# Performance work log

Hardware: AMD Instinct MI355X
Metric: run time of the kernel (lower is better)

Reference implementation:

```python
import jax, jax.numpy as jnp
import numpy as np

N = 3000
NFEAT = 512
NHID1 = 64
NHID2 = 32
FUS = 64
NCLASS = 8
NHEADS = 4
NADJ = 2
ALPHA = 0.2
NEG = -9e15


def setup_inputs() -> dict:
    key = jax.random.key(0)
    ks = jax.random.split(key, 14)
    s = 0.1
    return dict(
        x=jax.random.normal(ks[0], (N, NFEAT), jnp.float32),
        adj=jax.random.randint(ks[1], (NADJ, N, N), 0, 2, jnp.int32),
        W1=jax.random.normal(ks[2], (NADJ, NHEADS, NFEAT, NHID1), jnp.float32) * s,
        a1=jax.random.normal(ks[3], (NADJ, NHEADS, 2 * NHID1), jnp.float32) * s,
        W2=jax.random.normal(ks[4], (NADJ, NHEADS, FUS, NHID2), jnp.float32) * s,
        a2=jax.random.normal(ks[5], (NADJ, NHEADS, 2 * NHID2), jnp.float32) * s,
        wint1=jax.random.normal(ks[6], (FUS, NHID1 * NHEADS), jnp.float32) * s,
        bint1=jax.random.normal(ks[7], (FUS,), jnp.float32) * s,
        wfus1=jax.random.normal(ks[8], (FUS, FUS * NADJ), jnp.float32) * s,
        bfus1=jax.random.normal(ks[9], (FUS,), jnp.float32) * s,
        wint2=jax.random.normal(ks[10], (NCLASS, NHID2 * NHEADS), jnp.float32) * s,
        bint2=jax.random.normal(ks[11], (NCLASS,), jnp.float32) * s,
        wfus2=jax.random.normal(ks[12], (NCLASS, NCLASS * NADJ), jnp.float32) * s,
        bfus2=jax.random.normal(ks[13], (NCLASS,), jnp.float32) * s,
    )


def _gat(h, adj, W, a):
    # h: [N,F] shared input; W: [A,H,F,O]; a: [A,H,2O]; adj: [A,N,N]
    O = W.shape[-1]
    Wh = jnp.einsum('nf,ahfo->ahno', h, W)                 # [A,H,N,O]
    f1 = jnp.einsum('ahno,aho->ahn', Wh, a[..., :O])
    f2 = jnp.einsum('ahno,aho->ahn', Wh, a[..., O:])
    e = jax.nn.leaky_relu(f1[:, :, :, None] + f2[:, :, None, :], ALPHA)
    e = jnp.where(adj[:, None, :, :] > 0, e, NEG)          # masked scores
    att = jax.nn.softmax(e, axis=-1)                       # row softmax
    hp = jax.nn.elu(jnp.einsum('ahnm,ahmo->ahno', att, Wh))
    A, H, n, o = hp.shape
    return hp.transpose(0, 2, 1, 3).reshape(A, n, H * o)   # head concat: [A,N,H*O]


def reference(x, adj, W1, a1, W2, a2, wint1, bint1, wfus1, bfus1,
              wint2, bint2, wfus2, bfus2):
    # stage 1 (dropout is identity in eval mode)
    h1 = _gat(x, adj, W1, a1)                                      # [A,N,H*NHID1]
    h1 = jax.nn.elu(jnp.einsum('anf,gf->ang', h1, wint1) + bint1)  # [A,N,FUS]
    h1 = h1.transpose(1, 0, 2).reshape(h1.shape[1], -1)            # [N,A*FUS]
    out = h1 @ wfus1.T + bfus1                                     # [N,FUS]
    l1a = jnp.mean(jnp.abs(wfus1))
    # stage 2
    h2 = _gat(out, adj, W2, a2)                                    # [A,N,H*NHID2]
    h2 = jax.nn.elu(jnp.einsum('anf,gf->ang', h2, wint2) + bint2)  # [A,N,NCLASS]
    h2 = h2.transpose(1, 0, 2).reshape(h2.shape[1], -1)            # [N,A*NCLASS]
    out2 = h2 @ wfus2.T + bfus2                                    # [N,NCLASS]
    l1b = jnp.mean(jnp.abs(wfus2))
    return jax.nn.log_softmax(out2, axis=1), l1a + l1b
```

## Files before the change

kernel.cpp:

```cpp
#include <hip/hip_runtime.h>
#include <hip/hip_bf16.h>
#include <math.h>

#define NNODE 3000
#define NCHUNK 47
#define NBPR 376
#define ALPHA 0.2f
#define LDT 3008
#define LOG2E 1.4426950408889634f

typedef __attribute__((ext_vector_type(8))) short short8v;
typedef __attribute__((ext_vector_type(4))) short short4v;
typedef __attribute__((ext_vector_type(4))) float float4v;

static __device__ __forceinline__ short f2b(float x) {
  __hip_bfloat16 b = __float2bfloat16(x);
  return *reinterpret_cast<short*>(&b);
}
static __device__ __forceinline__ float b2f(unsigned short u) {
  unsigned v = ((unsigned)u) << 16;
  return *reinterpret_cast<float*>(&v);
}

__global__ __launch_bounds__(256)
void k_bitmask(const int* __restrict__ adj, unsigned char* __restrict__ bmb) {
  int idx = blockIdx.x * 256 + threadIdx.x;
  if (idx >= 2 * NNODE * NBPR) return;
  int row = idx / NBPR, b = idx % NBPR;
  unsigned char v = 0;
  if (b < 375) {
    const int* p = adj + (size_t)row * NNODE + 8 * b;
    int4 a0 = *reinterpret_cast<const int4*>(p);
    int4 a1 = *reinterpret_cast<const int4*>(p + 4);
    v = (unsigned char)((a0.x > 0) | ((a0.y > 0) << 1) | ((a0.z > 0) << 2) |
                        ((a0.w > 0) << 3) | ((a1.x > 0) << 4) | ((a1.y > 0) << 5) |
                        ((a1.z > 0) << 6) | ((a1.w > 0) << 7));
  }
  bmb[idx] = v;
}

__global__ __launch_bounds__(256)
void k_cast(const float* __restrict__ src, unsigned short* __restrict__ dst,
            int count8) {
  int i = blockIdx.x * 256 + threadIdx.x;
  if (i >= count8) return;
  float4 va = reinterpret_cast<const float4*>(src)[2 * i];
  float4 vb = reinterpret_cast<const float4*>(src)[2 * i + 1];
  short8v w;
  w[0] = f2b(va.x); w[1] = f2b(va.y); w[2] = f2b(va.z); w[3] = f2b(va.w);
  w[4] = f2b(vb.x); w[5] = f2b(vb.y); w[6] = f2b(vb.z); w[7] = f2b(vb.w);
  reinterpret_cast<short8v*>(dst)[i] = w;
}

template <int O>
__global__ __launch_bounds__(256)
void k_wt(const float* __restrict__ src, unsigned short* __restrict__ dst,
          int rows, int ldT) {
  const int z = blockIdx.y;
  const int m0 = blockIdx.x * 64;
  src += (size_t)z * rows * O;
  dst += (size_t)z * O * ldT;
  __shared__ float Lw[64][O + 4];
  const int tid = threadIdx.x;
  for (int idx = tid; idx < 64 * (O / 4); idx += 256) {
    int m = idx / (O / 4), oc = idx % (O / 4);
    float4 v = make_float4(0.f, 0.f, 0.f, 0.f);
    if (m0 + m < rows)
      v = *reinterpret_cast<const float4*>(&src[(size_t)(m0 + m) * O + 4 * oc]);
    *reinterpret_cast<float4*>(&Lw[m][4 * oc]) = v;
  }
  __syncthreads();
  const int o = tid & (O - 1);
  for (int mc = tid / O; mc < 8; mc += 256 / O) {
    short8v w;
#pragma unroll
    for (int j = 0; j < 8; ++j) w[j] = f2b(Lw[8 * mc + j][o]);
    *reinterpret_cast<short8v*>(&dst[(size_t)o * ldT + m0 + 8 * mc]) = w;
  }
}

template <int OW, int KC, int MODE, int ACT>
__global__ __launch_bounds__(128)
void k_xw(const unsigned short* __restrict__ Ab, long long boffA,
          const unsigned short* __restrict__ Bb, long long boffB,
          const float* __restrict__ aux,
          unsigned short* __restrict__ Wo,
          long long boffW,
          float* __restrict__ f1o, float* __restrict__ f2o,
          int colStrideZ, int ldC) {
  constexpr int NCT = OW / 16;
  const int z = blockIdx.z;
  const int n0 = blockIdx.x * 32;
  const int ocol0 = blockIdx.y * OW;
  const unsigned short* A = Ab + boffA * z;
  const unsigned short* B = Bb + boffB * z;
  const int tid = threadIdx.x;
  const int l = tid & 63, g = l >> 4, li = l & 15;
  const int r0 = 16 * (tid >> 6);
  __shared__ __align__(16) unsigned short As[32 * 64];
  __shared__ __align__(16) unsigned short Bs[OW * 64];
  float4v acc[NCT];
#pragma unroll
  for (int ct = 0; ct < NCT; ++ct) acc[ct] = {0.f, 0.f, 0.f, 0.f};
  for (int k0 = 0; k0 < KC; k0 += 64) {
    for (int i = tid; i < 256; i += 128) {
      int r = i >> 3, c8 = i & 7;
      uint4 v = {0u, 0u, 0u, 0u};
      if (n0 + r < NNODE)
        v = *reinterpret_cast<const uint4*>(A + (size_t)(n0 + r) * KC + k0 + 8 * c8);
      int boff = (r * 128 + c8 * 16) ^ ((r & 7) << 4);
      *reinterpret_cast<uint4*>(reinterpret_cast<char*>(As) + boff) = v;
    }
    for (int i = tid; i < OW * 8; i += 128) {
      int ro = i >> 3, c8 = i & 7;
      uint4 v = *reinterpret_cast<const uint4*>(B + (size_t)(ocol0 + ro) * KC + k0 + 8 * c8);
      int boff = (ro * 128 + c8 * 16) ^ ((ro & 7) << 4);
      *reinterpret_cast<uint4*>(reinterpret_cast<char*>(Bs) + boff) = v;
    }
    __syncthreads();
#pragma unroll
    for (int q = 0; q < 2; ++q) {
      int aoff = ((r0 + li) * 128 + q * 64 + 16 * g) ^ ((li & 7) << 4);
      short8v afr = *reinterpret_cast<const short8v*>(
          reinterpret_cast<const char*>(As) + aoff);
#pragma unroll
      for (int ct = 0; ct < NCT; ++ct) {
        int orow = ct * 16 + li;
        int boff = (orow * 128 + q * 64 + 16 * g) ^ ((li & 7) << 4);
        short8v bfr = *reinterpret_cast<const short8v*>(
            reinterpret_cast<const char*>(Bs) + boff);
        acc[ct] = __builtin_amdgcn_mfma_f32_16x16x32_bf16(afr, bfr, acc[ct], 0, 0, 0);
      }
    }
    __syncthreads();
  }
  if (MODE == 1) {
    const float* av = aux + (size_t)z * 2 * OW;
    float p1[4] = {0.f, 0.f, 0.f, 0.f}, p2[4] = {0.f, 0.f, 0.f, 0.f};
#pragma unroll
    for (int ct = 0; ct < NCT; ++ct) {
      float a1v = av[ct * 16 + li];
      float a2v = av[OW + ct * 16 + li];
#pragma unroll
      for (int j = 0; j < 4; ++j) {
        p1[j] += acc[ct][j] * a1v;
        p2[j] += acc[ct][j] * a2v;
      }
    }
#pragma unroll
    for (int off = 1; off < 16; off <<= 1) {
#pragma unroll
      for (int j = 0; j < 4; ++j) {
        p1[j] += __shfl_xor(p1[j], off);
        p2[j] += __shfl_xor(p2[j], off);
      }
    }
    unsigned short* WT = Wo + boffW * z;
#pragma unroll
    for (int ct = 0; ct < NCT; ++ct) {
      short4v w;
#pragma unroll
      for (int j = 0; j < 4; ++j) w[j] = f2b(acc[ct][j]);
      *reinterpret_cast<short4v*>(
          &WT[(size_t)(ocol0 + ct * 16 + li) * LDT + n0 + r0 + 4 * g]) = w;
    }
    if (li == 0) {
#pragma unroll
      for (int j = 0; j < 4; ++j) {
        int n = n0 + r0 + 4 * g + j;
        if (n < NNODE) {
          f1o[(size_t)z * NNODE + n] = p1[j] * LOG2E;
          f2o[(size_t)z * NNODE + n] = p2[j] * LOG2E;
        }
      }
    }
  } else {
#pragma unroll
    for (int ct = 0; ct < NCT; ++ct) {
      float b = aux[ocol0 + ct * 16 + li];
#pragma unroll
      for (int j = 0; j < 4; ++j) {
        int n = n0 + r0 + 4 * g + j;
        if (n < NNODE) {
          float v = acc[ct][j] + b;
          if (ACT == 1) v = v > 0.f ? v : (__expf(v) - 1.f);
          Wo[(size_t)n * ldC + z * colStrideZ + ocol0 + ct * 16 + li] = (unsigned short)f2b(v);
        }
      }
    }
  }
}

template <int O, int CPS, bool PB16>
__global__ __launch_bounds__(256)
void k_pvp(const unsigned short* __restrict__ WhT,
           const float* __restrict__ f1, const float* __restrict__ f2,
           const unsigned long long* __restrict__ bm,
           void* __restrict__ Cpart, float* __restrict__ rsum) {
  constexpr int NCT = O / 16;
  const int z = blockIdx.z, a = z >> 2;
  const int ks = blockIdx.y;
  const int n0 = blockIdx.x * 64;
  const int kc0 = ks * CPS;
  const int nch = (NCHUNK - kc0 < CPS) ? (NCHUNK - kc0) : CPS;
  const int tid = threadIdx.x;
  const int l = tid & 63, li = l & 15, g = l >> 4;
  const int r0 = 16 * (tid >> 6);
  const unsigned short* WT = WhT + (size_t)z * O * LDT;
  const float* f2B = f2 + (size_t)z * NNODE;
  const unsigned long long* bmA = bm + (size_t)a * NNODE * NCHUNK;
  __shared__ __align__(16) unsigned short Whs[2][O * 64];
  __shared__ __align__(16) float F2d[2][64];
  __shared__ unsigned long long Bw2[2][64];
  __shared__ float F1s[64];
  if (tid < 64) {
    int n = n0 + tid;
    F1s[tid] = (n < NNODE) ? f1[(size_t)z * NNODE + n] : 0.f;
  }
  short8v onesf;
  {
    short ov = (li == 0) ? (short)0x3F80 : (short)0;
#pragma unroll
    for (int e = 0; e < 8; ++e) onesf[e] = ov;
  }
  auto stage = [&](int t, int buf) {
    if (tid < 64) {
      int n = n0 + tid;
      Bw2[buf][tid] = (n < NNODE) ? bmA[(size_t)n * NCHUNK + kc0 + t] : 0ULL;
    } else if (tid < 128) {
      int m = (kc0 + t) * 64 + (tid - 64);
      F2d[buf][tid - 64] = (m < NNODE) ? f2B[m] : 0.f;
    }
    for (int i = tid; i < O * 8; i += 256) {
      int ro = i >> 3, c8 = i & 7;
      uint4 v = *reinterpret_cast<const uint4*>(
          WT + (size_t)ro * LDT + (size_t)(kc0 + t) * 64 + 8 * c8);
      int boff = (ro * 128 + c8 * 16) ^ ((ro & 7) << 4);
      *reinterpret_cast<uint4*>(reinterpret_cast<char*>(Whs[buf]) + boff) = v;
    }
  };
  float4v acc[NCT];
#pragma unroll
  for (int ct = 0; ct < NCT; ++ct) acc[ct] = {0.f, 0.f, 0.f, 0.f};
  float4v accs = {0.f, 0.f, 0.f, 0.f};
  stage(0, 0);
  __syncthreads();
  for (int t = 0; t < nch; ++t) {
    int buf = t & 1;
    if (t + 1 < nch) stage(t + 1, buf ^ 1);
    const unsigned long long bwr = Bw2[buf][r0 + li];
    const float f1v = F1s[r0 + li];
    short8v afr[2];
#pragma unroll
    for (int q = 0; q < 2; ++q) {
      int koff = 32 * q + 8 * g;
      unsigned bits = (unsigned)(bwr >> koff) & 0xffu;
      const float4 fa = *reinterpret_cast<const float4*>(&F2d[buf][koff]);
      const float4 fb = *reinterpret_cast<const float4*>(&F2d[buf][koff + 4]);
      float f2v[8] = {fa.x, fa.y, fa.z, fa.w, fb.x, fb.y, fb.z, fb.w};
#pragma unroll
      for (int e = 0; e < 8; ++e) {
        float tt = f1v + f2v[e];
        tt = fmaxf(tt, ALPHA * tt);
        tt = (bits & (1u << e)) ? tt : -1.0e30f;
        afr[q][e] = f2b(__builtin_amdgcn_exp2f(tt));
      }
    }
#pragma unroll
    for (int ct = 0; ct < NCT; ++ct) {
      int orow = ct * 16 + li;
#pragma unroll
      for (int q = 0; q < 2; ++q) {
        int boff = (orow * 128 + q * 64 + 16 * g) ^ ((li & 7) << 4);
        short8v bfr = *reinterpret_cast<const short8v*>(
            reinterpret_cast<const char*>(Whs[buf]) + boff);
        acc[ct] = __builtin_amdgcn_mfma_f32_16x16x32_bf16(afr[q], bfr, acc[ct], 0, 0, 0);
      }
    }
    accs = __builtin_amdgcn_mfma_f32_16x16x32_bf16(afr[0], onesf, accs, 0, 0, 0);
    accs = __builtin_amdgcn_mfma_f32_16x16x32_bf16(afr[1], onesf, accs, 0, 0, 0);
    __syncthreads();
  }
  if (PB16) {
    unsigned short* Cp = (unsigned short*)Cpart + ((size_t)ks * 8 + z) * NNODE * O;
#pragma unroll
    for (int j = 0; j < 4; ++j) {
      int n = n0 + r0 + 4 * g + j;
      if (n < NNODE) {
#pragma unroll
        for (int ct = 0; ct < NCT; ++ct)
          Cp[(size_t)n * O + ct * 16 + li] = (unsigned short)f2b(acc[ct][j]);
      }
    }
  } else {
    float* Cp = (float*)Cpart + ((size_t)ks * 8 + z) * NNODE * O;
#pragma unroll
    for (int j = 0; j < 4; ++j) {
      int n = n0 + r0 + 4 * g + j;
      if (n < NNODE) {
#pragma unroll
        for (int ct = 0; ct < NCT; ++ct)
          Cp[(size_t)n * O + ct * 16 + li] = acc[ct][j];
      }
    }
  }
  if (li == 0) {
#pragma unroll
    for (int j = 0; j < 4; ++j) {
      int n = n0 + r0 + 4 * g + j;
      if (n < NNODE) rsum[((size_t)ks * 8 + z) * NNODE + n] = accs[j];
    }
  }
}

template <int O, int KS, bool PB16, bool WB16>
__global__ __launch_bounds__(256)
void k_pvred(const void* __restrict__ Cpart, const float* __restrict__ rsum,
             float* __restrict__ Cf, unsigned short* __restrict__ Cb) {
  constexpr int C4 = O / 4;
  int idx = blockIdx.x * 256 + threadIdx.x;
  if (idx >= 8 * NNODE * C4) return;
  int zn = idx / C4, c4 = idx % C4;
  int z = zn / NNODE, n = zn % NNODE;
  int a = z >> 2, h = z & 3;
  float s = 0.f;
#pragma unroll
  for (int k = 0; k < KS; ++k) s += rsum[(size_t)k * 8 * NNODE + zn];
  float inv = (s > 0.f) ? 1.f / s : 0.f;
  float accv[4] = {0.f, 0.f, 0.f, 0.f};
#pragma unroll
  for (int k = 0; k < KS; ++k) {
    if (PB16) {
      short4v v = *reinterpret_cast<const short4v*>(
          (const unsigned short*)Cpart + (size_t)k * 8 * NNODE * O + (size_t)zn * O + 4 * c4);
#pragma unroll
      for (int j = 0; j < 4; ++j) accv[j] += b2f((unsigned short)v[j]);
    } else {
      float4 v = *reinterpret_cast<const float4*>(
          (const float*)Cpart + (size_t)k * 8 * NNODE * O + (size_t)zn * O + 4 * c4);
      accv[0] += v.x; accv[1] += v.y; accv[2] += v.z; accv[3] += v.w;
    }
  }
  size_t base = ((size_t)a * NNODE + n) * (4 * O) + (size_t)h * O + 4 * c4;
  if (WB16) {
    short4v w;
#pragma unroll
    for (int j = 0; j < 4; ++j) {
      float v = accv[j] * inv;
      v = v > 0.f ? v : (__expf(v) - 1.f);
      w[j] = f2b(v);
    }
    *reinterpret_cast<short4v*>(Cb + base) = w;
  } else {
    float4 w;
    float* wp = &w.x;
#pragma unroll
    for (int j = 0; j < 4; ++j) {
      float v = accv[j] * inv;
      wp[j] = v > 0.f ? v : (__expf(v) - 1.f);
    }
    *reinterpret_cast<float4*>(Cf + base) = w;
  }
}

template <int BM, int BN, int BK, int TM, int TN, bool BT, int ACT>
__global__ __launch_bounds__((BM / TM) * (BN / TN))
void k_gemm(const float* __restrict__ A, long long boffA, int ldA,
            const float* __restrict__ B, long long boffB,
            const float* __restrict__ bias,
            float* __restrict__ C, long long boffC, int ldC,
            int M, int N, int K) {
  constexpr int NT = (BM / TM) * (BN / TN);
  constexpr int NCG = BN / TN;
  const int z = blockIdx.z;
  A += boffA * z;
  B += boffB * z;
  C += boffC * z;
  const int m0 = blockIdx.x * BM;
  const int n0 = blockIdx.y * BN;
  __shared__ float As[BK][BM + 4];
  __shared__ float Bs[BK][BN + 4];
  const int tid = threadIdx.x;
  const int trow = tid / NCG, tcol = tid % NCG;
  float acc[TM][TN] = {};
  for (int k0 = 0; k0 < K; k0 += BK) {
    for (int i = tid; i < BM * BK; i += NT) {
      int r = i / BK, c = i % BK;
      int gm = m0 + r;
      As[c][r] = (gm < M) ? A[(size_t)gm * ldA + (k0 + c)] : 0.f;
    }
    if (!BT) {
      for (int i = tid; i < BK * BN; i += NT) {
        int r = i / BN, c = i % BN;
        Bs[r][c] = B[(size_t)(k0 + r) * N + (n0 + c)];
      }
    } else {
      for (int i = tid; i < BK * BN; i += NT) {
        int r = i % BK, c = i / BK;
        Bs[r][c] = B[(size_t)(n0 + c) * K + (k0 + r)];
      }
    }
    __syncthreads();
#pragma unroll 8
    for (int kk = 0; kk < BK; ++kk) {
      float ar[TM], br[TN];
#pragma unroll
      for (int i2 = 0; i2 < TM; ++i2) ar[i2] = As[kk][trow * TM + i2];
#pragma unroll
      for (int j = 0; j < TN; ++j) br[j] = Bs[kk][tcol * TN + j];
#pragma unroll
      for (int i2 = 0; i2 < TM; ++i2)
#pragma unroll
        for (int j = 0; j < TN; ++j)
          acc[i2][j] = fmaf(ar[i2], br[j], acc[i2][j]);
    }
    __syncthreads();
  }
#pragma unroll
  for (int i2 = 0; i2 < TM; ++i2) {
    int gm = m0 + trow * TM + i2;
    if (gm >= M) continue;
#pragma unroll
    for (int j = 0; j < TN; ++j) {
      int gn = n0 + tcol * TN + j;
      float v = acc[i2][j];
      if (bias) v += bias[gn];
      if (ACT == 1) v = v > 0.f ? v : (__expf(v) - 1.f);
      C[(size_t)gm * ldC + gn] = v;
    }
  }
}

__global__ __launch_bounds__(256)
void k_lsm(const float* __restrict__ out2, float* __restrict__ out) {
  int n = blockIdx.x * blockDim.x + threadIdx.x;
  if (n >= NNODE) return;
  const float* r = out2 + (size_t)n * 8;
  float mx = r[0];
#pragma unroll
  for (int j = 1; j < 8; ++j) mx = fmaxf(mx, r[j]);
  float s = 0.f;
#pragma unroll
  for (int j = 0; j < 8; ++j) s += __expf(r[j] - mx);
  float ls = __logf(s) + mx;
#pragma unroll
  for (int j = 0; j < 8; ++j) out[(size_t)n * 8 + j] = r[j] - ls;
}

__global__ __launch_bounds__(256)
void k_l1(const float* __restrict__ wfus1, const float* __restrict__ wfus2,
          float* __restrict__ o) {
  __shared__ float red[256];
  int tid = threadIdx.x;
  float s1 = 0.f, s2 = 0.f;
  for (int i = tid; i < 64 * 128; i += 256) s1 += fabsf(wfus1[i]);
  if (tid < 128) s2 = fabsf(wfus2[tid]);
  red[tid] = s1 / 8192.f + s2 / 128.f;
  __syncthreads();
  for (int off = 128; off; off >>= 1) {
    if (tid < off) red[tid] += red[tid + off];
    __syncthreads();
  }
  if (tid == 0) o[0] = red[0];
}

extern "C" void kernel_launch(void* const* d_in, const int* in_sizes, int n_in,
                              void* d_out, int out_size, void* d_ws, size_t ws_size,
                              hipStream_t stream) {
  const float* x = (const float*)d_in[0];
  const int* adj = (const int*)d_in[1];
  const float* W1 = (const float*)d_in[2];
  const float* a1 = (const float*)d_in[3];
  const float* W2 = (const float*)d_in[4];
  const float* a2 = (const float*)d_in[5];
  const float* wint1 = (const float*)d_in[6];
  const float* bint1 = (const float*)d_in[7];
  const float* wfus1 = (const float*)d_in[8];
  const float* bfus1 = (const float*)d_in[9];
  const float* wint2 = (const float*)d_in[10];
  const float* bint2 = (const float*)d_in[11];
  const float* wfus2 = (const float*)d_in[12];
  const float* bfus2 = (const float*)d_in[13];
  float* out = (float*)d_out;

  float* W = (float*)d_ws;
  unsigned long long* bm = (unsigned long long*)d_ws;
  unsigned short* xb = (unsigned short*)(W + 564000);
  unsigned short* h1catb = (unsigned short*)(W + 564000);
  float* h2cat = W + 564000;
  unsigned short* W1Tb = (unsigned short*)(W + 1332000);
  unsigned short* wint1b = (unsigned short*)(W + 1463072);
  unsigned short* wfus1b = (unsigned short*)(W + 1471264);
  unsigned short* W2Tb = (unsigned short*)(W + 1475360);
  float* f1b = W + 1483552;
  float* f2g = W + 1507552;
  unsigned short* WhT1 = (unsigned short*)(W + 1531552);
  unsigned short* t1b = (unsigned short*)(W + 1531552);
  unsigned short* out1b = (unsigned short*)(W + 1723552);
  unsigned short* WhT2 = (unsigned short*)(W + 1819552);
  float* t2 = W + 2301600;
  float* out2 = W + 2349600;
  float* rsumw = W + 2373600;
  void* Cpart = (void*)(W + 2469600);

  k_bitmask<<<dim3((2 * NNODE * NBPR + 255) / 256), 256, 0, stream>>>(
      adj, (unsigned char*)bm);
  k_cast<<<dim3(750), 256, 0, stream>>>(x, xb, 192000);
  k_wt<64><<<dim3(8, 8), 256, 0, stream>>>(W1, W1Tb, 512, 512);
  k_cast<<<dim3(8), 256, 0, stream>>>(wint1, wint1b, 2048);
  k_cast<<<dim3(4), 256, 0, stream>>>(wfus1, wfus1b, 1024);
  k_wt<32><<<dim3(1, 8), 256, 0, stream>>>(W2, W2Tb, 64, 64);

  k_xw<64, 512, 1, 0><<<dim3(94, 1, 8), 128, 0, stream>>>(
      xb, 0, W1Tb, 64 * 512, a1, WhT1, (long long)64 * LDT, f1b, f2g, 0, 0);
  k_pvp<64, 12, true><<<dim3(47, 4, 8), 256, 0, stream>>>(WhT1, f1b, f2g, bm, Cpart, rsumw);
  k_pvred<64, 4, true, true><<<dim3(1500), 256, 0, stream>>>(Cpart, rsumw, nullptr, h1catb);
  k_xw<32, 256, 0, 1><<<dim3(94, 2, 2), 128, 0, stream>>>(
      h1catb, (long long)NNODE * 256, wint1b, 0, bint1, t1b, 0, nullptr, nullptr, 64, 128);
  k_xw<32, 128, 0, 0><<<dim3(94, 2, 1), 128, 0, stream>>>(
      t1b, 0, wfus1b, 0, bfus1, out1b, 0, nullptr, nullptr, 0, 64);

  k_xw<32, 64, 1, 0><<<dim3(94, 1, 8), 128, 0, stream>>>(
      out1b, 0, W2Tb, 32 * 64, a2, WhT2, (long long)32 * LDT, f1b, f2g, 0, 0);
  k_pvp<32, 12, false><<<dim3(47, 4, 8), 256, 0, stream>>>(WhT2, f1b, f2g, bm, Cpart, rsumw);
  k_pvred<32, 4, false, false><<<dim3(750), 256, 0, stream>>>(Cpart, rsumw, h2cat, nullptr);

  k_gemm<32, 8, 32, 2, 1, true, 1><<<dim3(94, 1, 2), 128, 0, stream>>>(
      h2cat, (long long)NNODE * 128, 128, wint2, 0, bint2, t2, 8, 16, NNODE, 8, 128);
  k_gemm<32, 8, 16, 2, 1, true, 0><<<dim3(94, 1, 1), 128, 0, stream>>>(
      t2, 0, 16, wfus2, 0, bfus2, out2, 0, 8, NNODE, 8, 16);

  k_lsm<<<dim3((NNODE + 255) / 256), 256, 0, stream>>>(out2, out);
  k_l1<<<dim3(1), 256, 0, stream>>>(wfus1, wfus2, out + 24000);
}
```

Before: 164.0 us.

## Fuse preprocessing kernels into one launch and fuse stage-2 tail into one kernel

Six small preprocessing kernels (adjacency bitmask, bf16 casts of x and weights, weight transposes) become one block-range-dispatched kernel. The tail is also merged: the two small GEMMs, the log-softmax and the L1 reduction now run in one kernel. Each wave handles one node using shuffle reductions, and the t2/out2 intermediates no longer round-trip through global memory. This cuts kernel-launch and inter-kernel gap overhead, at the cost of one kernel with mixed block roles and shared-memory sizing set by the largest role.

Result: faster. 136.6 us (-16.7%).

```diff
diff --git a/kernel.cpp b/kernel.cpp
--- a/kernel.cpp
+++ b/kernel.cpp
@@ -22,28 +22,16 @@
   return *reinterpret_cast<float*>(&v);
 }
 
-__global__ __launch_bounds__(256)
-void k_bitmask(const int* __restrict__ adj, unsigned char* __restrict__ bmb) {
-  int idx = blockIdx.x * 256 + threadIdx.x;
-  if (idx >= 2 * NNODE * NBPR) return;
-  int row = idx / NBPR, b = idx % NBPR;
-  unsigned char v = 0;
-  if (b < 375) {
-    const int* p = adj + (size_t)row * NNODE + 8 * b;
-    int4 a0 = *reinterpret_cast<const int4*>(p);
-    int4 a1 = *reinterpret_cast<const int4*>(p + 4);
-    v = (unsigned char)((a0.x > 0) | ((a0.y > 0) << 1) | ((a0.z > 0) << 2) |
-                        ((a0.w > 0) << 3) | ((a1.x > 0) << 4) | ((a1.y > 0) << 5) |
-                        ((a1.z > 0) << 6) | ((a1.w > 0) << 7));
-  }
-  bmb[idx] = v;
-}
-
-__global__ __launch_bounds__(256)
-void k_cast(const float* __restrict__ src, unsigned short* __restrict__ dst,
-            int count8) {
-  int i = blockIdx.x * 256 + threadIdx.x;
-  if (i >= count8) return;
+#define PB_BM 8813
+#define PB_XC 750
+#define PB_W1 64
+#define PB_WI 8
+#define PB_WF 4
+#define PB_W2 8
+#define PREP_BLOCKS (PB_BM + PB_XC + PB_W1 + PB_WI + PB_WF + PB_W2)
+
+static __device__ __forceinline__ void cast8(const float* __restrict__ src,
+                                             unsigned short* __restrict__ dst, int i) {
   float4 va = reinterpret_cast<const float4*>(src)[2 * i];
   float4 vb = reinterpret_cast<const float4*>(src)[2 * i + 1];
   short8v w;
@@ -52,30 +40,69 @@
   reinterpret_cast<short8v*>(dst)[i] = w;
 }
 
-template <int O>
-__global__ __launch_bounds__(256)
-void k_wt(const float* __restrict__ src, unsigned short* __restrict__ dst,
-          int rows, int ldT) {
-  const int z = blockIdx.y;
-  const int m0 = blockIdx.x * 64;
-  src += (size_t)z * rows * O;
-  dst += (size_t)z * O * ldT;
-  __shared__ float Lw[64][O + 4];
+static __device__ void wt_body(const float* __restrict__ src,
+                               unsigned short* __restrict__ dst,
+                               int rows, int O, int ldT, int m0, float* Lw) {
   const int tid = threadIdx.x;
-  for (int idx = tid; idx < 64 * (O / 4); idx += 256) {
-    int m = idx / (O / 4), oc = idx % (O / 4);
+  const int ocnt = O / 4;
+  for (int idx = tid; idx < 64 * ocnt; idx += 256) {
+    int m = idx / ocnt, oc = idx % ocnt;
     float4 v = make_float4(0.f, 0.f, 0.f, 0.f);
     if (m0 + m < rows)
       v = *reinterpret_cast<const float4*>(&src[(size_t)(m0 + m) * O + 4 * oc]);
-    *reinterpret_cast<float4*>(&Lw[m][4 * oc]) = v;
+    *reinterpret_cast<float4*>(&Lw[m * 68 + 4 * oc]) = v;
   }
   __syncthreads();
   const int o = tid & (O - 1);
   for (int mc = tid / O; mc < 8; mc += 256 / O) {
     short8v w;
 #pragma unroll
-    for (int j = 0; j < 8; ++j) w[j] = f2b(Lw[8 * mc + j][o]);
+    for (int j = 0; j < 8; ++j) w[j] = f2b(Lw[(8 * mc + j) * 68 + o]);
     *reinterpret_cast<short8v*>(&dst[(size_t)o * ldT + m0 + 8 * mc]) = w;
+  }
+}
+
+__global__ __launch_bounds__(256)
+void k_prep(const int* __restrict__ adj, unsigned char* __restrict__ bmb,
+            const float* __restrict__ x, unsigned short* __restrict__ xb,
+            const float* __restrict__ W1, unsigned short* __restrict__ W1Tb,
+            const float* __restrict__ wint1, unsigned short* __restrict__ wint1b,
+            const float* __restrict__ wfus1, unsigned short* __restrict__ wfus1b,
+            const float* __restrict__ W2, unsigned short* __restrict__ W2Tb) {
+  __shared__ float Lw[64 * 68];
+  const int b = blockIdx.x;
+  const int tid = threadIdx.x;
+  if (b < PB_BM) {
+    int idx = b * 256 + tid;
+    if (idx < 2 * NNODE * NBPR) {
+      int row = idx / NBPR, by = idx % NBPR;
+      unsigned char v = 0;
+      if (by < 375) {
+        const int* p = adj + (size_t)row * NNODE + 8 * by;
+        int4 a0 = *reinterpret_cast<const int4*>(p);
+        int4 a1 = *reinterpret_cast<const int4*>(p + 4);
+        v = (unsigned char)((a0.x > 0) | ((a0.y > 0) << 1) | ((a0.z > 0) << 2) |
+                            ((a0.w > 0) << 3) | ((a1.x > 0) << 4) | ((a1.y > 0) << 5) |
+                            ((a1.z > 0) << 6) | ((a1.w > 0) << 7));
+      }
+      bmb[idx] = v;
+    }
+  } else if (b < PB_BM + PB_XC) {
+    int i = (b - PB_BM) * 256 + tid;
+    if (i < 192000) cast8(x, xb, i);
+  } else if (b < PB_BM + PB_XC + PB_W1) {
+    int zb = b - (PB_BM + PB_XC);
+    int z = zb >> 3, m0 = (zb & 7) * 64;
+    wt_body(W1 + (size_t)z * 512 * 64, W1Tb + (size_t)z * 64 * 512, 512, 64, 512, m0, Lw);
+  } else if (b < PB_BM + PB_XC + PB_W1 + PB_WI) {
+    int i = (b - (PB_BM + PB_XC + PB_W1)) * 256 + tid;
+    if (i < 2048) cast8(wint1, wint1b, i);
+  } else if (b < PB_BM + PB_XC + PB_W1 + PB_WI + PB_WF) {
+    int i = (b - (PB_BM + PB_XC + PB_W1 + PB_WI)) * 256 + tid;
+    if (i < 1024) cast8(wfus1, wfus1b, i);
+  } else {
+    int z = b - (PB_BM + PB_XC + PB_W1 + PB_WI + PB_WF);
+    wt_body(W2 + (size_t)z * 64 * 32, W2Tb + (size_t)z * 32 * 64, 64, 32, 64, 0, Lw);
   }
 }
 
@@ -363,105 +390,64 @@
   }
 }
 
-template <int BM, int BN, int BK, int TM, int TN, bool BT, int ACT>
-__global__ __launch_bounds__((BM / TM) * (BN / TN))
-void k_gemm(const float* __restrict__ A, long long boffA, int ldA,
-            const float* __restrict__ B, long long boffB,
-            const float* __restrict__ bias,
-            float* __restrict__ C, long long boffC, int ldC,
-            int M, int N, int K) {
-  constexpr int NT = (BM / TM) * (BN / TN);
-  constexpr int NCG = BN / TN;
-  const int z = blockIdx.z;
-  A += boffA * z;
-  B += boffB * z;
-  C += boffC * z;
-  const int m0 = blockIdx.x * BM;
-  const int n0 = blockIdx.y * BN;
-  __shared__ float As[BK][BM + 4];
-  __shared__ float Bs[BK][BN + 4];
+__global__ __launch_bounds__(256)
+void k_tail(const float* __restrict__ h2cat, const float* __restrict__ wint2,
+            const float* __restrict__ bint2, const float* __restrict__ wfus2,
+            const float* __restrict__ bfus2, const float* __restrict__ wfus1,
+            float* __restrict__ out) {
   const int tid = threadIdx.x;
-  const int trow = tid / NCG, tcol = tid % NCG;
-  float acc[TM][TN] = {};
-  for (int k0 = 0; k0 < K; k0 += BK) {
-    for (int i = tid; i < BM * BK; i += NT) {
-      int r = i / BK, c = i % BK;
-      int gm = m0 + r;
-      As[c][r] = (gm < M) ? A[(size_t)gm * ldA + (k0 + c)] : 0.f;
-    }
-    if (!BT) {
-      for (int i = tid; i < BK * BN; i += NT) {
-        int r = i / BN, c = i % BN;
-        Bs[r][c] = B[(size_t)(k0 + r) * N + (n0 + c)];
-      }
-    } else {
-      for (int i = tid; i < BK * BN; i += NT) {
-        int r = i % BK, c = i / BK;
-        Bs[r][c] = B[(size_t)(n0 + c) * K + (k0 + r)];
-      }
-    }
+  if (blockIdx.x == 750) {
+    __shared__ float red[256];
+    float s1 = 0.f, s2 = 0.f;
+    for (int i = tid; i < 64 * 128; i += 256) s1 += fabsf(wfus1[i]);
+    if (tid < 128) s2 = fabsf(wfus2[tid]);
+    red[tid] = s1 / 8192.f + s2 / 128.f;
     __syncthreads();
-#pragma unroll 8
-    for (int kk = 0; kk < BK; ++kk) {
-      float ar[TM], br[TN];
-#pragma unroll
-      for (int i2 = 0; i2 < TM; ++i2) ar[i2] = As[kk][trow * TM + i2];
-#pragma unroll
-      for (int j = 0; j < TN; ++j) br[j] = Bs[kk][tcol * TN + j];
-#pragma unroll
-      for (int i2 = 0; i2 < TM; ++i2)
-#pragma unroll
-        for (int j = 0; j < TN; ++j)
-          acc[i2][j] = fmaf(ar[i2], br[j], acc[i2][j]);
-    }
-    __syncthreads();
-  }
-#pragma unroll
-  for (int i2 = 0; i2 < TM; ++i2) {
-    int gm = m0 + trow * TM + i2;
-    if (gm >= M) continue;
-#pragma unroll
-    for (int j = 0; j < TN; ++j) {
-      int gn = n0 + tcol * TN + j;
-      float v = acc[i2][j];
-      if (bias) v += bias[gn];
-      if (ACT == 1) v = v > 0.f ? v : (__expf(v) - 1.f);
-      C[(size_t)gm * ldC + gn] = v;
-    }
-  }
-}
-
-__global__ __launch_bounds__(256)
-void k_lsm(const float* __restrict__ out2, float* __restrict__ out) {
-  int n = blockIdx.x * blockDim.x + threadIdx.x;
-  if (n >= NNODE) return;
-  const float* r = out2 + (size_t)n * 8;
-  float mx = r[0];
-#pragma unroll
-  for (int j = 1; j < 8; ++j) mx = fmaxf(mx, r[j]);
+    for (int off = 128; off; off >>= 1) {
+      if (tid < off) red[tid] += red[tid + off];
+      __syncthreads();
+    }
+    if (tid == 0) out[24000] = red[0];
+    return;
+  }
+  __shared__ float T2s[4][16];
+  const int w = tid >> 6, l = tid & 63;
+  const int n = blockIdx.x * 4 + w;
+  const int o = l & 15, q = l >> 4;
+  const int zz = o >> 3, c = o & 7;
+  const float* ar = h2cat + (size_t)zz * NNODE * 128 + (size_t)n * 128 + q * 32;
+  const float* wr = wint2 + (size_t)c * 128 + q * 32;
   float s = 0.f;
 #pragma unroll
-  for (int j = 0; j < 8; ++j) s += __expf(r[j] - mx);
-  float ls = __logf(s) + mx;
-#pragma unroll
-  for (int j = 0; j < 8; ++j) out[(size_t)n * 8 + j] = r[j] - ls;
-}
-
-__global__ __launch_bounds__(256)
-void k_l1(const float* __restrict__ wfus1, const float* __restrict__ wfus2,
-          float* __restrict__ o) {
-  __shared__ float red[256];
-  int tid = threadIdx.x;
-  float s1 = 0.f, s2 = 0.f;
-  for (int i = tid; i < 64 * 128; i += 256) s1 += fabsf(wfus1[i]);
-  if (tid < 128) s2 = fabsf(wfus2[tid]);
-  red[tid] = s1 / 8192.f + s2 / 128.f;
-  __syncthreads();
-  for (int off = 128; off; off >>= 1) {
-    if (tid < off) red[tid] += red[tid + off];
-    __syncthreads();
-  }
-  if (tid == 0) o[0] = red[0];
+  for (int i = 0; i < 8; ++i) {
+    float4 av = *reinterpret_cast<const float4*>(ar + 4 * i);
+    float4 wv = *reinterpret_cast<const float4*>(wr + 4 * i);
+    s = fmaf(av.x, wv.x, s); s = fmaf(av.y, wv.y, s);
+    s = fmaf(av.z, wv.z, s); s = fmaf(av.w, wv.w, s);
+  }
+  s += __shfl_xor(s, 16);
+  s += __shfl_xor(s, 32);
+  if (q == 0) {
+    float v = s + bint2[c];
+    v = v > 0.f ? v : (__expf(v) - 1.f);
+    T2s[w][o] = v;
+  }
+  if (l < 8) {
+    float v = bfus2[l];
+#pragma unroll
+    for (int k = 0; k < 16; ++k) v = fmaf(T2s[w][k], wfus2[l * 16 + k], v);
+    float mx = v;
+    mx = fmaxf(mx, __shfl_xor(mx, 1, 8));
+    mx = fmaxf(mx, __shfl_xor(mx, 2, 8));
+    mx = fmaxf(mx, __shfl_xor(mx, 4, 8));
+    float ex = __expf(v - mx);
+    float sm = ex;
+    sm += __shfl_xor(sm, 1, 8);
+    sm += __shfl_xor(sm, 2, 8);
+    sm += __shfl_xor(sm, 4, 8);
+    float ls = __logf(sm) + mx;
+    out[(size_t)n * 8 + l] = v - ls;
+  }
 }
 
 extern "C" void kernel_launch(void* const* d_in, const int* in_sizes, int n_in,
@@ -498,18 +484,11 @@
   unsigned short* t1b = (unsigned short*)(W + 1531552);
   unsigned short* out1b = (unsigned short*)(W + 1723552);
   unsigned short* WhT2 = (unsigned short*)(W + 1819552);
-  float* t2 = W + 2301600;
-  float* out2 = W + 2349600;
   float* rsumw = W + 2373600;
   void* Cpart = (void*)(W + 2469600);
 
-  k_bitmask<<<dim3((2 * NNODE * NBPR + 255) / 256), 256, 0, stream>>>(
-      adj, (unsigned char*)bm);
-  k_cast<<<dim3(750), 256, 0, stream>>>(x, xb, 192000);
-  k_wt<64><<<dim3(8, 8), 256, 0, stream>>>(W1, W1Tb, 512, 512);
-  k_cast<<<dim3(8), 256, 0, stream>>>(wint1, wint1b, 2048);
-  k_cast<<<dim3(4), 256, 0, stream>>>(wfus1, wfus1b, 1024);
-  k_wt<32><<<dim3(1, 8), 256, 0, stream>>>(W2, W2Tb, 64, 64);
+  k_prep<<<dim3(PREP_BLOCKS), 256, 0, stream>>>(
+      adj, (unsigned char*)bm, x, xb, W1, W1Tb, wint1, wint1b, wfus1, wfus1b, W2, W2Tb);
 
   k_xw<64, 512, 1, 0><<<dim3(94, 1, 8), 128, 0, stream>>>(
       xb, 0, W1Tb, 64 * 512, a1, WhT1, (long long)64 * LDT, f1b, f2g, 0, 0);
@@ -525,11 +504,5 @@
   k_pvp<32, 12, false><<<dim3(47, 4, 8), 256, 0, stream>>>(WhT2, f1b, f2g, bm, Cpart, rsumw);
   k_pvred<32, 4, false, false><<<dim3(750), 256, 0, stream>>>(Cpart, rsumw, h2cat, nullptr);
 
-  k_gemm<32, 8, 32, 2, 1, true, 1><<<dim3(94, 1, 2), 128, 0, stream>>>(
-      h2cat, (long long)NNODE * 128, 128, wint2, 0, bint2, t2, 8, 16, NNODE, 8, 128);
-  k_gemm<32, 8, 16, 2, 1, true, 0><<<dim3(94, 1, 1), 128, 0, stream>>>(
-      t2, 0, 16, wfus2, 0, bfus2, out2, 0, 8, NNODE, 8, 16);
-
-  k_lsm<<<dim3((NNODE + 255) / 256), 256, 0, stream>>>(out2, out);
-  k_l1<<<dim3(1), 256, 0, stream>>>(wfus1, wfus2, out + 24000);
-}
+  k_tail<<<dim3(751), 256, 0, stream>>>(h2cat, wint2, bint2, wfus2, bfus2, wfus1, out);
+}
```
